# Kernel optimization log

Hardware: AMD Instinct MI355X
Metric: run time of the kernel (lower is better)

## Reference

```python
import jax, jax.numpy as jnp
import numpy as np

N = 100000   # nodes
E = 1600000  # edges
D = 128      # in = hid = out feature dim
EPS = 1e-5


def gcn_conv(x, W, b, src, dst, w, n):
    # PyG GCNConv: h = x W; symmetric normalization with self-loops already in (src,dst,w)
    h = x @ W                                        # [N, D]
    deg = jax.ops.segment_sum(w, dst, num_segments=n)
    dinv = jnp.where(deg > 0, deg ** -0.5, 0.0)
    norm = dinv[src] * w * dinv[dst]                 # [E+N]
    out = jax.ops.segment_sum(h[src] * norm[:, None], dst, num_segments=n)
    return out + b


def batch_norm(x, gamma, beta):
    m = x.mean(axis=0)
    v = x.var(axis=0)  # biased, as PyTorch uses for normalization
    return gamma * (x - m) * jax.lax.rsqrt(v + EPS) + beta


def setup_inputs() -> dict:
    key = jax.random.key(0)
    ks = jax.random.split(key, 10)
    x = jax.random.normal(ks[0], (N, D), dtype=jnp.float32)
    edge_index = jax.random.randint(ks[1], (2, E), 0, N, dtype=jnp.int64)
    edge_weight = jax.random.uniform(ks[2], (E,), dtype=jnp.float32)
    s = 1.0 / np.sqrt(D)
    W1 = jax.random.uniform(ks[3], (D, D), jnp.float32, -s, s)
    b1 = jax.random.uniform(ks[4], (D,), jnp.float32, -s, s)
    W2 = jax.random.uniform(ks[5], (D, D), jnp.float32, -s, s)
    b2 = jax.random.uniform(ks[6], (D,), jnp.float32, -s, s)
    g1 = jnp.ones((D,), jnp.float32); beta1 = jnp.zeros((D,), jnp.float32)
    g2 = jnp.ones((D,), jnp.float32); beta2 = jnp.zeros((D,), jnp.float32)
    return {"x": x, "edge_index": edge_index, "edge_weight": edge_weight,
            "W1": W1, "b1": b1, "W2": W2, "b2": b2,
            "g1": g1, "beta1": beta1, "g2": g2, "beta2": beta2}


def reference(x, edge_index, edge_weight, W1, b1, W2, b2, g1, beta1, g2, beta2):
    loops = jnp.arange(N, dtype=edge_index.dtype)
    src = jnp.concatenate([edge_index[0], loops])
    dst = jnp.concatenate([edge_index[1], loops])
    w = jnp.concatenate([edge_weight, jnp.ones((N,), edge_weight.dtype)])
    # layer 1: GCNConv -> BN -> relu (dropout inactive in eval)
    h = gcn_conv(x, W1, b1, src, dst, w, N)
    h = jax.nn.relu(batch_norm(h, g1, beta1))
    # layer 2
    h = gcn_conv(h, W2, b2, src, dst, w, N)
    h = jax.nn.relu(batch_norm(h, g2, beta2))
    return h
```

## Files before the change

### kernel.cpp

```cpp
#include <hip/hip_runtime.h>
#include <hip/hip_bf16.h>

#define NN 100000
#define EE 1600000
#define DD 128
#define CAP 56
#define NB 391
#define CAPB 6144
#define NRG 6250
#define NC 16
#define BN_EPS 1e-5f

typedef __attribute__((ext_vector_type(8))) short short8;
typedef __attribute__((ext_vector_type(4))) float f32x4;
typedef __attribute__((ext_vector_type(4))) unsigned int u32x4;

__device__ __forceinline__ float bfu2f(unsigned short u) {
    return __uint_as_float(((unsigned int)u) << 16);
}
__device__ __forceinline__ unsigned short f2bfu(float f) {
    unsigned int u = __float_as_uint(f);
    unsigned int r = (u + 0x7fffu + ((u >> 16) & 1u)) >> 16;
    return (unsigned short)r;
}
__device__ __forceinline__ void atomAddF(float* p, float v) {
    unsafeAtomicAdd(p, v);
}
__device__ __forceinline__ float ldF(const void* __restrict__ p, int isf32, size_t idx) {
    return isf32 ? ((const float*)p)[idx]
                 : bfu2f(((const unsigned short*)p)[idx]);
}
__device__ __forceinline__ int edge_at(const int* __restrict__ ei, int is64, unsigned int pos) {
    return is64 ? ei[(size_t)pos * 2] : ei[pos];
}

__global__ __launch_bounds__(256) void prep2(const int* __restrict__ ei,
                                             const unsigned int* __restrict__ g1w,
                                             const void* __restrict__ W1,
                                             const void* __restrict__ W2,
                                             int* __restrict__ flags,
                                             unsigned int* __restrict__ cursor,
                                             float* __restrict__ stats,
                                             unsigned short* __restrict__ Wt1,
                                             unsigned short* __restrict__ Wt2) {
    int t = threadIdx.x;
    int b = blockIdx.x;
    int isf32 = (g1w[0] == 0x3F800000u) ? 1 : 0;
    if (b == 0) {
        __shared__ int nz;
        if (t == 0) nz = 0;
        __syncthreads();
        if (ei[2 * t + 1] != 0) atomicExch(&nz, 1);
        __syncthreads();
        if (t == 0) {
            flags[0] = (nz == 0) ? 1 : 0;
            flags[1] = isf32;
        }
        stats[t] = 0.f;
        stats[512 + t] = 0.f;
    } else if (b == 129) {
        for (int i = t; i < 512; i += 256) cursor[i] = 0;
    } else {
        int i = (b - 1) * 256 + t;
        if (i < 16384) {
            int r = i >> 7, c = i & 127;
            Wt1[c * DD + r] = f2bfu(ldF(W1, isf32, i));
        } else {
            int j = i - 16384;
            int r = j >> 7, c = j & 127;
            Wt2[c * DD + r] = f2bfu(ldF(W2, isf32, j));
        }
    }
}

__device__ __forceinline__ void load_arow(const void* __restrict__ Xv, int isf32,
                                          int row, int quad, short8* dst) {
#pragma unroll
    for (int k4 = 0; k4 < 4; ++k4) {
        int k = k4 * 32 + quad * 8;
        if (isf32) {
            const float* xf = (const float*)Xv + (size_t)row * DD + k;
            float4 f0 = *(const float4*)xf;
            float4 f1 = *(const float4*)(xf + 4);
            short8 a;
            a[0] = (short)f2bfu(f0.x); a[1] = (short)f2bfu(f0.y);
            a[2] = (short)f2bfu(f0.z); a[3] = (short)f2bfu(f0.w);
            a[4] = (short)f2bfu(f1.x); a[5] = (short)f2bfu(f1.y);
            a[6] = (short)f2bfu(f1.z); a[7] = (short)f2bfu(f1.w);
            dst[k4] = a;
        } else {
            dst[k4] = *(const short8*)((const short*)Xv + (size_t)row * DD + k);
        }
    }
}

__global__ __launch_bounds__(256) void fatk(const void* __restrict__ Xv,
                                            const int* __restrict__ flags,
                                            const unsigned short* __restrict__ Wt,
                                            unsigned short* __restrict__ H,
                                            const int* __restrict__ ei,
                                            const void* __restrict__ w,
                                            uint2* __restrict__ staging,
                                            unsigned int* __restrict__ cursor) {
    __shared__ __align__(16) float lc[4][16][36];
    unsigned int g = blockIdx.x;
    unsigned int q = g / 3u, r = g % 3u;
    if (r == 2u) {
        __shared__ unsigned int cnt[NB], base[NB];
        for (int i = threadIdx.x; i < NB; i += 256) cnt[i] = 0;
        __syncthreads();
        int is64 = flags[0], isf32 = flags[1];
        unsigned int e0 = q * 2048u;
        unsigned int lo[8], hi[8], rk[8];
        int bk[8];
#pragma unroll
        for (int i = 0; i < 8; ++i) {
            unsigned int e = e0 + i * 256u + threadIdx.x;
            bk[i] = -1;
            if (e < EE) {
                int s = edge_at(ei, is64, e);
                int d = edge_at(ei, is64, EE + e);
                float wv = ldF(w, isf32, e);
                unsigned int wfix = __float2uint_rn(wv * 16777216.0f);
                wfix = wfix > 0xFFFFFFu ? 0xFFFFFFu : wfix;
                lo[i] = ((unsigned int)f2bfu(wv) << 17) | (unsigned int)s;
                hi[i] = (wfix << 8) | (unsigned int)(d & 255);
                bk[i] = d >> 8;
                rk[i] = atomicAdd(&cnt[bk[i]], 1u);
            }
        }
        __syncthreads();
        for (int i = threadIdx.x; i < NB; i += 256)
            base[i] = cnt[i] ? atomicAdd(&cursor[i], cnt[i]) : 0u;
        __syncthreads();
#pragma unroll
        for (int i = 0; i < 8; ++i) {
            if (bk[i] >= 0) {
                unsigned int pos = base[bk[i]] + rk[i];
                if (pos < CAPB)
                    staging[(size_t)bk[i] * CAPB + pos] = make_uint2(lo[i], hi[i]);
            }
        }
    } else {
        int gid = (int)(q * 2u + r);
        int isf32 = flags[1];
        int lane = threadIdx.x & 63;
        int wave = threadIdx.x >> 6;
        int m = lane & 15, quad = lane >> 4;
        int orow = lane >> 2, ocq = lane & 3;
        int n0 = wave * 32;
        const short* Ws = (const short*)Wt;
        short8 B0[4], B1[4];
#pragma unroll
        for (int k4 = 0; k4 < 4; ++k4) {
            int k = k4 * 32 + quad * 8;
            B0[k4] = *(const short8*)(Ws + (size_t)(n0 + m) * DD + k);
            B1[k4] = *(const short8*)(Ws + (size_t)(n0 + 16 + m) * DD + k);
        }
        int rgbase = gid * 4;
        short8 aC[4], aN[4];
        int rg0 = min(rgbase, NRG - 1);
        load_arow(Xv, isf32, rg0 * 16 + m, quad, aC);
#pragma unroll
        for (int rg = 0; rg < 4; ++rg) {
            int rgg = min(rgbase + rg, NRG - 1);
            if (rg < 3) {
                int rgn = min(rgbase + rg + 1, NRG - 1);
                load_arow(Xv, isf32, rgn * 16 + m, quad, aN);
            }
            f32x4 acc0 = {0.f, 0.f, 0.f, 0.f};
            f32x4 acc1 = {0.f, 0.f, 0.f, 0.f};
#pragma unroll
            for (int k4 = 0; k4 < 4; ++k4) {
                acc0 = __builtin_amdgcn_mfma_f32_16x16x32_bf16(aC[k4], B0[k4], acc0, 0, 0, 0);
                acc1 = __builtin_amdgcn_mfma_f32_16x16x32_bf16(aC[k4], B1[k4], acc1, 0, 0, 0);
            }
#pragma unroll
            for (int rr = 0; rr < 4; ++rr) {
                lc[wave][quad * 4 + rr][m]      = acc0[rr];
                lc[wave][quad * 4 + rr][16 + m] = acc1[rr];
            }
            float4 c0 = *(const float4*)&lc[wave][orow][ocq * 8];
            float4 c1 = *(const float4*)&lc[wave][orow][ocq * 8 + 4];
            short8 o;
            o[0] = (short)f2bfu(c0.x); o[1] = (short)f2bfu(c0.y);
            o[2] = (short)f2bfu(c0.z); o[3] = (short)f2bfu(c0.w);
            o[4] = (short)f2bfu(c1.x); o[5] = (short)f2bfu(c1.y);
            o[6] = (short)f2bfu(c1.z); o[7] = (short)f2bfu(c1.w);
            int row0 = rgg * 16;
            *(short8*)(H + (size_t)(row0 + orow) * DD + n0 + ocq * 8) = o;
#pragma unroll
            for (int k4 = 0; k4 < 4; ++k4) aC[k4] = aN[k4];
        }
    }
}

__global__ __launch_bounds__(256) void ellbuild(const uint2* __restrict__ staging,
                                                const unsigned int* __restrict__ cursor,
                                                unsigned int* __restrict__ ell,
                                                unsigned long long* __restrict__ meta,
                                                float* __restrict__ gacc) {
    __shared__ __align__(16) unsigned int lrow[256 * CAP];
    __shared__ unsigned int lcnt[256], lws[256];
    int b = blockIdx.x, t = threadIdx.x;
    if (b < 32) gacc[b * 256 + t] = 0.f;
    lcnt[t] = 0; lws[t] = 0;
    {
        uint4 z = make_uint4(0, 0, 0, 0);
        uint4* lp = (uint4*)lrow;
        for (int j = t; j < 256 * CAP / 4; j += 256) lp[j] = z;
    }
    __syncthreads();
    unsigned int rc = cursor[b];
    if (rc > CAPB) rc = CAPB;
    const uint2* S = staging + (size_t)b * CAPB;
    for (unsigned int j = t; j < rc; j += 256) {
        uint2 rec = S[j];
        unsigned int dl = rec.y & 255u;
        unsigned int rk = atomicAdd(&lcnt[dl], 1u);
        atomicAdd(&lws[dl], rec.y >> 8);
        if (rk < CAP) lrow[dl * CAP + rk] = rec.x;
    }
    __syncthreads();
    int nrows = NN - b * 256;
    if (nrows > 256) nrows = 256;
    int nv = nrows * (CAP / 4);
    uint4* dst = (uint4*)(ell + (size_t)b * 256 * CAP);
    const uint4* src = (const uint4*)lrow;
    for (int j = t; j < nv; j += 256) {
        int r = j / 14, c = j - r * 14;
        unsigned int c8r = (lcnt[r] + 7u) & ~7u;
        if (c8r > CAP) c8r = CAP;
        if ((unsigned int)(c * 4) < c8r) dst[j] = src[j];
    }
    if (t < nrows) {
        unsigned int c = lcnt[t];
        unsigned int c8 = (c + 7u) & ~7u;
        if (c8 > CAP) c8 = CAP;
        float dv = rsqrtf(1.0f + (float)lws[t] * (1.0f / 16777216.0f));
        meta[b * 256 + t] = ((unsigned long long)c8 << 32) |
                            (unsigned long long)__float_as_uint(dv);
    }
}

template <int PREMUL>
__device__ __forceinline__ void proc4(u32x4 qv, const float* __restrict__ dvp,
                                      const unsigned short* __restrict__ Hf,
                                      float& a0, float& a1, float& a2, float& a3) {
    unsigned int qa[4] = {qv.x, qv.y, qv.z, qv.w};
#pragma unroll
    for (int t = 0; t < 4; ++t) {
        unsigned int ent = qa[t];
        int s = (int)(ent & 0x1FFFFu);
        float wv = __uint_as_float((ent >> 1) & 0xFFFF0000u);
        float we = PREMUL ? wv : wv * dvp[2 * s];
        ushort4 h = *(const ushort4*)(Hf + ((size_t)s << 7));
        a0 = fmaf(bfu2f(h.x), we, a0);
        a1 = fmaf(bfu2f(h.y), we, a1);
        a2 = fmaf(bfu2f(h.z), we, a2);
        a3 = fmaf(bfu2f(h.w), we, a3);
    }
}

template <int PREMUL>
__global__ __launch_bounds__(256) void gather_agg(const unsigned short* __restrict__ H,
                                                  const unsigned long long* __restrict__ meta,
                                                  const unsigned int* __restrict__ ell,
                                                  unsigned short* __restrict__ A,
                                                  float* __restrict__ gacc) {
    __shared__ float lsum[4][128], lss[4][128];
    int wave = threadIdx.x >> 6;
    int lane = threadIdx.x & 63;
    int half = lane >> 5;
    int sub = lane & 31;
    const unsigned short* Hf = H + sub * 4;
    const float* dvp = (const float*)meta;
    float sv0 = 0.f, sv1 = 0.f, sv2 = 0.f, sv3 = 0.f;
    float sq0 = 0.f, sq1 = 0.f, sq2 = 0.f, sq3 = 0.f;
#pragma unroll
    for (int u = 0; u < 2; ++u) {
        int n = blockIdx.x * 8 + wave * 2 + u;
        unsigned long long m = meta[n];
        int cnt8 = (int)(m >> 32);
        float di = __uint_as_float((unsigned int)m);
        float a0 = 0.f, a1 = 0.f, a2 = 0.f, a3 = 0.f;
        if (half == 0) {
            ushort4 hs = *(const ushort4*)(Hf + ((size_t)n << 7));
            if (PREMUL) {
                a0 = bfu2f(hs.x); a1 = bfu2f(hs.y);
                a2 = bfu2f(hs.z); a3 = bfu2f(hs.w);
            } else {
                a0 = bfu2f(hs.x) * di; a1 = bfu2f(hs.y) * di;
                a2 = bfu2f(hs.z) * di; a3 = bfu2f(hs.w) * di;
            }
        }
        const unsigned int* row = ell + (size_t)n * CAP + (half << 2);
        if (cnt8 > 0) {
            u32x4 qc = __builtin_nontemporal_load((const u32x4*)row);
            u32x4 qn = __builtin_nontemporal_load((const u32x4*)(row + 8));
            for (int i = 0; i + 8 < cnt8; i += 8) {
                u32x4 qf = __builtin_nontemporal_load((const u32x4*)(row + i + 16));
                proc4<PREMUL>(qc, dvp, Hf, a0, a1, a2, a3);
                qc = qn; qn = qf;
            }
            proc4<PREMUL>(qc, dvp, Hf, a0, a1, a2, a3);
        }
        a0 += __shfl_down(a0, 32);
        a1 += __shfl_down(a1, 32);
        a2 += __shfl_down(a2, 32);
        a3 += __shfl_down(a3, 32);
        if (half == 0) {
            ushort4 o;
            o.x = f2bfu(a0 * di);
            o.y = f2bfu(a1 * di);
            o.z = f2bfu(a2 * di);
            o.w = f2bfu(a3 * di);
            *(ushort4*)(A + ((size_t)n << 7) + sub * 4) = o;
            float v0 = bfu2f(o.x), v1 = bfu2f(o.y), v2 = bfu2f(o.z), v3 = bfu2f(o.w);
            sv0 += v0; sv1 += v1; sv2 += v2; sv3 += v3;
            sq0 += v0 * v0; sq1 += v1 * v1; sq2 += v2 * v2; sq3 += v3 * v3;
        }
    }
    if (half == 0) {
        int fb = sub * 4;
        lsum[wave][fb + 0] = sv0; lsum[wave][fb + 1] = sv1;
        lsum[wave][fb + 2] = sv2; lsum[wave][fb + 3] = sv3;
        lss[wave][fb + 0] = sq0; lss[wave][fb + 1] = sq1;
        lss[wave][fb + 2] = sq2; lss[wave][fb + 3] = sq3;
    }
    __syncthreads();
    int t = threadIdx.x;
    if (t < 128) {
        float s = lsum[0][t] + lsum[1][t] + lsum[2][t] + lsum[3][t];
        float q = lss[0][t] + lss[1][t] + lss[2][t] + lss[3][t];
        float* gb = gacc + (blockIdx.x & (NC - 1)) * 256;
        atomAddF(&gb[t], s);
        atomAddF(&gb[128 + t], q);
    }
}

__global__ __launch_bounds__(256) void gemm2(const unsigned short* __restrict__ A,
                                             const float* __restrict__ scale,
                                             const float* __restrict__ shift,
                                             const unsigned short* __restrict__ Wt,
                                             const unsigned long long* __restrict__ meta,
                                             unsigned short* __restrict__ H) {
    __shared__ __align__(16) float lsc[DD], lsh[DD];
    __shared__ __align__(16) float lc[4][16][36];
    if (threadIdx.x < DD) {
        lsc[threadIdx.x] = scale[threadIdx.x];
        lsh[threadIdx.x] = shift[threadIdx.x];
    }
    __syncthreads();
    int lane = threadIdx.x & 63;
    int wave = threadIdx.x >> 6;
    int m = lane & 15, quad = lane >> 4;
    int orow = lane >> 2, ocq = lane & 3;
    int n0 = wave * 32;
    const short* Ws = (const short*)Wt;
    const float* dvp = (const float*)meta;
    short8 B0[4], B1[4];
#pragma unroll
    for (int k4 = 0; k4 < 4; ++k4) {
        int k = k4 * 32 + quad * 8;
        B0[k4] = *(const short8*)(Ws + (size_t)(n0 + m) * DD + k);
        B1[k4] = *(const short8*)(Ws + (size_t)(n0 + 16 + m) * DD + k);
    }
    int rgbase = blockIdx.x * 4;
    short8 aC[4], aN[4];
#define LOADA2(dst, RG)                                                           \
    {                                                                             \
        int rr_ = (RG) * 16 + m;                                                  \
        const short* ap_ = (const short*)A + (size_t)rr_ * DD;                    \
        _Pragma("unroll")                                                         \
        for (int k4_ = 0; k4_ < 4; ++k4_) {                                       \
            int k_ = k4_ * 32 + quad * 8;                                         \
            short8 raw_ = *(const short8*)(ap_ + k_);                             \
            float4 sc0_ = *(const float4*)(lsc + k_);                             \
            float4 sc1_ = *(const float4*)(lsc + k_ + 4);                         \
            float4 sh0_ = *(const float4*)(lsh + k_);                             \
            float4 sh1_ = *(const float4*)(lsh + k_ + 4);                         \
            short8 a_;                                                            \
            a_[0] = (short)f2bfu(fmaxf(fmaf(bfu2f((unsigned short)raw_[0]), sc0_.x, sh0_.x), 0.f)); \
            a_[1] = (short)f2bfu(fmaxf(fmaf(bfu2f((unsigned short)raw_[1]), sc0_.y, sh0_.y), 0.f)); \
            a_[2] = (short)f2bfu(fmaxf(fmaf(bfu2f((unsigned short)raw_[2]), sc0_.z, sh0_.z), 0.f)); \
            a_[3] = (short)f2bfu(fmaxf(fmaf(bfu2f((unsigned short)raw_[3]), sc0_.w, sh0_.w), 0.f)); \
            a_[4] = (short)f2bfu(fmaxf(fmaf(bfu2f((unsigned short)raw_[4]), sc1_.x, sh1_.x), 0.f)); \
            a_[5] = (short)f2bfu(fmaxf(fmaf(bfu2f((unsigned short)raw_[5]), sc1_.y, sh1_.y), 0.f)); \
            a_[6] = (short)f2bfu(fmaxf(fmaf(bfu2f((unsigned short)raw_[6]), sc1_.z, sh1_.z), 0.f)); \
            a_[7] = (short)f2bfu(fmaxf(fmaf(bfu2f((unsigned short)raw_[7]), sc1_.w, sh1_.w), 0.f)); \
            dst[k4_] = a_;                                                        \
        }                                                                         \
    }
    int rg0 = min(rgbase, NRG - 1);
    LOADA2(aC, rg0);
#pragma unroll
    for (int rg = 0; rg < 4; ++rg) {
        int rgg = min(rgbase + rg, NRG - 1);
        if (rg < 3) {
            int rgn = min(rgbase + rg + 1, NRG - 1);
            LOADA2(aN, rgn);
        }
        f32x4 acc0 = {0.f, 0.f, 0.f, 0.f};
        f32x4 acc1 = {0.f, 0.f, 0.f, 0.f};
#pragma unroll
        for (int k4 = 0; k4 < 4; ++k4) {
            acc0 = __builtin_amdgcn_mfma_f32_16x16x32_bf16(aC[k4], B0[k4], acc0, 0, 0, 0);
            acc1 = __builtin_amdgcn_mfma_f32_16x16x32_bf16(aC[k4], B1[k4], acc1, 0, 0, 0);
        }
#pragma unroll
        for (int rr = 0; rr < 4; ++rr) {
            lc[wave][quad * 4 + rr][m]      = acc0[rr];
            lc[wave][quad * 4 + rr][16 + m] = acc1[rr];
        }
        int row0 = rgg * 16;
        float dv = dvp[2 * (row0 + orow)];
        float4 c0 = *(const float4*)&lc[wave][orow][ocq * 8];
        float4 c1 = *(const float4*)&lc[wave][orow][ocq * 8 + 4];
        short8 o;
        o[0] = (short)f2bfu(c0.x * dv); o[1] = (short)f2bfu(c0.y * dv);
        o[2] = (short)f2bfu(c0.z * dv); o[3] = (short)f2bfu(c0.w * dv);
        o[4] = (short)f2bfu(c1.x * dv); o[5] = (short)f2bfu(c1.y * dv);
        o[6] = (short)f2bfu(c1.z * dv); o[7] = (short)f2bfu(c1.w * dv);
        *(short8*)(H + (size_t)(row0 + orow) * DD + n0 + ocq * 8) = o;
#pragma unroll
        for (int k4 = 0; k4 < 4; ++k4) aC[k4] = aN[k4];
    }
#undef LOADA2
}

__global__ __launch_bounds__(128) void bn_final(const float* __restrict__ gacc,
                                                const void* __restrict__ gamma,
                                                const void* __restrict__ beta,
                                                const int* __restrict__ flags,
                                                float* __restrict__ scale,
                                                float* __restrict__ shift) {
    int f = threadIdx.x;
    int isf32 = flags[1];
    float s = 0.f, ss = 0.f;
#pragma unroll
    for (int c = 0; c < NC; ++c) {
        s  += gacc[c * 256 + f];
        ss += gacc[c * 256 + 128 + f];
    }
    float m = s * (1.0f / NN);
    float v = ss * (1.0f / NN) - m * m;
    v = fmaxf(v, 0.0f);
    float sc = ldF(gamma, isf32, f) * rsqrtf(v + BN_EPS);
    scale[f] = sc;
    shift[f] = ldF(beta, isf32, f) - m * sc;
}

__global__ __launch_bounds__(256) void bn_apply(const unsigned short* __restrict__ A,
                                                const float* __restrict__ scale,
                                                const float* __restrict__ shift,
                                                const int* __restrict__ flags,
                                                void* __restrict__ out) {
    int i = blockIdx.x * 256 + threadIdx.x;
    int f = (i & 31) * 4;
    ushort4 v4 = ((const ushort4*)A)[i];
    float r0 = fmaxf(fmaf(bfu2f(v4.x), scale[f + 0], shift[f + 0]), 0.f);
    float r1 = fmaxf(fmaf(bfu2f(v4.y), scale[f + 1], shift[f + 1]), 0.f);
    float r2 = fmaxf(fmaf(bfu2f(v4.z), scale[f + 2], shift[f + 2]), 0.f);
    float r3 = fmaxf(fmaf(bfu2f(v4.w), scale[f + 3], shift[f + 3]), 0.f);
    if (flags[1]) {
        ((float4*)out)[i] = make_float4(r0, r1, r2, r3);
    } else {
        ushort4 o;
        o.x = f2bfu(r0); o.y = f2bfu(r1); o.z = f2bfu(r2); o.w = f2bfu(r3);
        ((ushort4*)out)[i] = o;
    }
}

extern "C" void kernel_launch(void* const* d_in, const int* in_sizes, int n_in,
                              void* d_out, int out_size, void* d_ws, size_t ws_size,
                              hipStream_t stream) {
    const void* x   = d_in[0];
    const int*  ei  = (const int*)d_in[1];
    const void* ew  = d_in[2];
    const void* W1  = d_in[3];
    const void* W2  = d_in[5];
    const void* g1  = d_in[7];
    const void* be1 = d_in[8];
    const void* g2  = d_in[9];
    const void* be2 = d_in[10];

    char* ws = (char*)d_ws;
    float* stats         = (float*)ws;
    int*   flags         = (int*)(ws + 4096);
    unsigned short* Wt1  = (unsigned short*)(ws + 4224);
    unsigned short* Wt2  = (unsigned short*)(ws + 36992);
    unsigned long long* meta = (unsigned long long*)(ws + 69760);
    unsigned int* ell    = (unsigned int*)(ws + 869760);
    unsigned short* Hbuf = (unsigned short*)(ws + 23269760);
    unsigned short* A    = (unsigned short*)(ws + 48869760);
    uint2* staging       = (uint2*)(ws + 48869760);
    unsigned int* cursor = (unsigned int*)(ws + 48869760 + 19218432);
    float* gaccL1 = (float*)(ws + 4224);
    float* gaccL2 = (float*)(ws + 4224 + 16384);
    float* scale1 = stats + 256, *shift1 = stats + 384;
    float* scale2 = stats + 768, *shift2 = stats + 896;

    prep2<<<130, 256, 0, stream>>>(ei, (const unsigned int*)g1, W1, W2,
                                   flags, cursor, stats, Wt1, Wt2);

    fatk<<<2346, 256, 0, stream>>>(x, flags, Wt1, Hbuf, ei, ew, staging, cursor);
    ellbuild<<<NB, 256, 0, stream>>>(staging, cursor, ell, meta, gaccL1);
    gather_agg<0><<<12500, 256, 0, stream>>>(Hbuf, meta, ell, A, gaccL1);
    bn_final<<<1, 128, 0, stream>>>(gaccL1, g1, be1, flags, scale1, shift1);

    gemm2<<<1563, 256, 0, stream>>>(A, scale1, shift1, Wt2, meta, Hbuf);
    gather_agg<1><<<12500, 256, 0, stream>>>(Hbuf, meta, ell, A, gaccL2);
    bn_final<<<1, 128, 0, stream>>>(gaccL2, g2, be2, flags, scale2, shift2);
    bn_apply<<<12500, 256, 0, stream>>>(A, scale2, shift2, flags, d_out);
}
```

Measured before the change: 355.8 us.

## Fold BN finalize into consumer kernels and deepen A-row prefetch in fatk

Removes the two single-block bn_final launches by having each block of gemm2 and bn_apply reduce the per-chunk BN partial sums into LDS scale/shift itself. bn_apply becomes a grid-stride kernel with 2048 blocks reading scale/shift from LDS instead of global memory. The fatk GEMM path now prefetches two row groups ahead instead of one, which uses more registers. The aim is to cut launch and serialization overhead, at the cost of redundant per-block reduction work.

Result: no change. 358.7 us (+0.8%).

```diff
diff --git a/kernel.cpp b/kernel.cpp
--- a/kernel.cpp
+++ b/kernel.cpp
@@ -34,13 +34,36 @@
     return is64 ? ei[(size_t)pos * 2] : ei[pos];
 }
 
+__device__ __forceinline__ void bn_reduce_lds(const float* __restrict__ gacc,
+                                              const void* __restrict__ gamma,
+                                              const void* __restrict__ beta,
+                                              const int* __restrict__ flags,
+                                              float* __restrict__ lsc,
+                                              float* __restrict__ lsh) {
+    int f = threadIdx.x;
+    if (f < 128) {
+        int isf32 = flags[1];
+        float s = 0.f, ss = 0.f;
+#pragma unroll
+        for (int c = 0; c < NC; ++c) {
+            s  += gacc[c * 256 + f];
+            ss += gacc[c * 256 + 128 + f];
+        }
+        float m = s * (1.0f / NN);
+        float v = ss * (1.0f / NN) - m * m;
+        v = fmaxf(v, 0.0f);
+        float sc = ldF(gamma, isf32, f) * rsqrtf(v + BN_EPS);
+        lsc[f] = sc;
+        lsh[f] = ldF(beta, isf32, f) - m * sc;
+    }
+}
+
 __global__ __launch_bounds__(256) void prep2(const int* __restrict__ ei,
                                              const unsigned int* __restrict__ g1w,
                                              const void* __restrict__ W1,
                                              const void* __restrict__ W2,
                                              int* __restrict__ flags,
                                              unsigned int* __restrict__ cursor,
-                                             float* __restrict__ stats,
                                              unsigned short* __restrict__ Wt1,
                                              unsigned short* __restrict__ Wt2) {
     int t = threadIdx.x;
@@ -56,8 +79,6 @@
             flags[0] = (nz == 0) ? 1 : 0;
             flags[1] = isf32;
         }
-        stats[t] = 0.f;
-        stats[512 + t] = 0.f;
     } else if (b == 129) {
         for (int i = t; i < 512; i += 256) cursor[i] = 0;
     } else {
@@ -158,15 +179,15 @@
             B1[k4] = *(const short8*)(Ws + (size_t)(n0 + 16 + m) * DD + k);
         }
         int rgbase = gid * 4;
-        short8 aC[4], aN[4];
-        int rg0 = min(rgbase, NRG - 1);
-        load_arow(Xv, isf32, rg0 * 16 + m, quad, aC);
+        short8 aC[4], aN[4], aM[4];
+        load_arow(Xv, isf32, min(rgbase, NRG - 1) * 16 + m, quad, aC);
+        load_arow(Xv, isf32, min(rgbase + 1, NRG - 1) * 16 + m, quad, aN);
 #pragma unroll
         for (int rg = 0; rg < 4; ++rg) {
             int rgg = min(rgbase + rg, NRG - 1);
-            if (rg < 3) {
-                int rgn = min(rgbase + rg + 1, NRG - 1);
-                load_arow(Xv, isf32, rgn * 16 + m, quad, aN);
+            if (rg < 2) {
+                int rgn = min(rgbase + rg + 2, NRG - 1);
+                load_arow(Xv, isf32, rgn * 16 + m, quad, aM);
             }
             f32x4 acc0 = {0.f, 0.f, 0.f, 0.f};
             f32x4 acc1 = {0.f, 0.f, 0.f, 0.f};
@@ -190,7 +211,7 @@
             int row0 = rgg * 16;
             *(short8*)(H + (size_t)(row0 + orow) * DD + n0 + ocq * 8) = o;
 #pragma unroll
-            for (int k4 = 0; k4 < 4; ++k4) aC[k4] = aN[k4];
+            for (int k4 = 0; k4 < 4; ++k4) { aC[k4] = aN[k4]; aN[k4] = aM[k4]; }
         }
     }
 }
@@ -340,17 +361,16 @@
 }
 
 __global__ __launch_bounds__(256) void gemm2(const unsigned short* __restrict__ A,
-                                             const float* __restrict__ scale,
-                                             const float* __restrict__ shift,
+                                             const float* __restrict__ gacc,
+                                             const void* __restrict__ gamma,
+                                             const void* __restrict__ beta,
+                                             const int* __restrict__ flags,
                                              const unsigned short* __restrict__ Wt,
                                              const unsigned long long* __restrict__ meta,
                                              unsigned short* __restrict__ H) {
     __shared__ __align__(16) float lsc[DD], lsh[DD];
     __shared__ __align__(16) float lc[4][16][36];
-    if (threadIdx.x < DD) {
-        lsc[threadIdx.x] = scale[threadIdx.x];
-        lsh[threadIdx.x] = shift[threadIdx.x];
-    }
+    bn_reduce_lds(gacc, gamma, beta, flags, lsc, lsh);
     __syncthreads();
     int lane = threadIdx.x & 63;
     int wave = threadIdx.x >> 6;
@@ -429,46 +449,30 @@
 #undef LOADA2
 }
 
-__global__ __launch_bounds__(128) void bn_final(const float* __restrict__ gacc,
+__global__ __launch_bounds__(256) void bn_apply(const unsigned short* __restrict__ A,
+                                                const float* __restrict__ gacc,
                                                 const void* __restrict__ gamma,
                                                 const void* __restrict__ beta,
                                                 const int* __restrict__ flags,
-                                                float* __restrict__ scale,
-                                                float* __restrict__ shift) {
-    int f = threadIdx.x;
+                                                void* __restrict__ out) {
+    __shared__ __align__(16) float lsc[DD], lsh[DD];
+    bn_reduce_lds(gacc, gamma, beta, flags, lsc, lsh);
+    __syncthreads();
     int isf32 = flags[1];
-    float s = 0.f, ss = 0.f;
-#pragma unroll
-    for (int c = 0; c < NC; ++c) {
-        s  += gacc[c * 256 + f];
-        ss += gacc[c * 256 + 128 + f];
-    }
-    float m = s * (1.0f / NN);
-    float v = ss * (1.0f / NN) - m * m;
-    v = fmaxf(v, 0.0f);
-    float sc = ldF(gamma, isf32, f) * rsqrtf(v + BN_EPS);
-    scale[f] = sc;
-    shift[f] = ldF(beta, isf32, f) - m * sc;
-}
-
-__global__ __launch_bounds__(256) void bn_apply(const unsigned short* __restrict__ A,
-                                                const float* __restrict__ scale,
-                                                const float* __restrict__ shift,
-                                                const int* __restrict__ flags,
-                                                void* __restrict__ out) {
-    int i = blockIdx.x * 256 + threadIdx.x;
-    int f = (i & 31) * 4;
-    ushort4 v4 = ((const ushort4*)A)[i];
-    float r0 = fmaxf(fmaf(bfu2f(v4.x), scale[f + 0], shift[f + 0]), 0.f);
-    float r1 = fmaxf(fmaf(bfu2f(v4.y), scale[f + 1], shift[f + 1]), 0.f);
-    float r2 = fmaxf(fmaf(bfu2f(v4.z), scale[f + 2], shift[f + 2]), 0.f);
-    float r3 = fmaxf(fmaf(bfu2f(v4.w), scale[f + 3], shift[f + 3]), 0.f);
-    if (flags[1]) {
-        ((float4*)out)[i] = make_float4(r0, r1, r2, r3);
-    } else {
-        ushort4 o;
-        o.x = f2bfu(r0); o.y = f2bfu(r1); o.z = f2bfu(r2); o.w = f2bfu(r3);
-        ((ushort4*)out)[i] = o;
+    for (int i = blockIdx.x * 256 + threadIdx.x; i < NN * 32; i += gridDim.x * 256) {
+        int f = (i & 31) * 4;
+        ushort4 v4 = ((const ushort4*)A)[i];
+        float r0 = fmaxf(fmaf(bfu2f(v4.x), lsc[f + 0], lsh[f + 0]), 0.f);
+        float r1 = fmaxf(fmaf(bfu2f(v4.y), lsc[f + 1], lsh[f + 1]), 0.f);
+        float r2 = fmaxf(fmaf(bfu2f(v4.z), lsc[f + 2], lsh[f + 2]), 0.f);
+        float r3 = fmaxf(fmaf(bfu2f(v4.w), lsc[f + 3], lsh[f + 3]), 0.f);
+        if (isf32) {
+            ((float4*)out)[i] = make_float4(r0, r1, r2, r3);
+        } else {
+            ushort4 o;
+            o.x = f2bfu(r0); o.y = f2bfu(r1); o.z = f2bfu(r2); o.w = f2bfu(r3);
+            ((ushort4*)out)[i] = o;
+        }
     }
 }
 
@@ -486,7 +490,6 @@
     const void* be2 = d_in[10];
 
     char* ws = (char*)d_ws;
-    float* stats         = (float*)ws;
     int*   flags         = (int*)(ws + 4096);
     unsigned short* Wt1  = (unsigned short*)(ws + 4224);
     unsigned short* Wt2  = (unsigned short*)(ws + 36992);
@@ -498,19 +501,15 @@
     unsigned int* cursor = (unsigned int*)(ws + 48869760 + 19218432);
     float* gaccL1 = (float*)(ws + 4224);
     float* gaccL2 = (float*)(ws + 4224 + 16384);
-    float* scale1 = stats + 256, *shift1 = stats + 384;
-    float* scale2 = stats + 768, *shift2 = stats + 896;
 
     prep2<<<130, 256, 0, stream>>>(ei, (const unsigned int*)g1, W1, W2,
-                                   flags, cursor, stats, Wt1, Wt2);
+                                   flags, cursor, Wt1, Wt2);
 
     fatk<<<2346, 256, 0, stream>>>(x, flags, Wt1, Hbuf, ei, ew, staging, cursor);
     ellbuild<<<NB, 256, 0, stream>>>(staging, cursor, ell, meta, gaccL1);
     gather_agg<0><<<12500, 256, 0, stream>>>(Hbuf, meta, ell, A, gaccL1);
-    bn_final<<<1, 128, 0, stream>>>(gaccL1, g1, be1, flags, scale1, shift1);
-
-    gemm2<<<1563, 256, 0, stream>>>(A, scale1, shift1, Wt2, meta, Hbuf);
+
+    gemm2<<<1563, 256, 0, stream>>>(A, gaccL1, g1, be1, flags, Wt2, meta, Hbuf);
     gather_agg<1><<<12500, 256, 0, stream>>>(Hbuf, meta, ell, A, gaccL2);
-    bn_final<<<1, 128, 0, stream>>>(gaccL2, g2, be2, flags, scale2, shift2);
-    bn_apply<<<12500, 256, 0, stream>>>(A, scale2, shift2, flags, d_out);
-}
+    bn_apply<<<2048, 256, 0, stream>>>(A, gaccL2, g2, be2, flags, d_out);
+}
```
